# Kernel tuning notes

Measured on AMD Instinct MI355X. Metric: run time of the kernel, lower is better.

The kernel has to match this reference:

```python
import jax, jax.numpy as jnp
import numpy as np

N_NODES = 100000
N_EDGES = 600000
D_FEAT = 128
N_CLASSES = 40
K = 2


def setup_inputs() -> dict:
    key = jax.random.key(0)
    k1, k2, k3, k4, k5 = jax.random.split(key, 5)
    x = jax.random.normal(k1, (N_NODES, D_FEAT), dtype=jnp.float32)
    edge_index = jax.random.randint(k2, (2, N_EDGES), 0, N_NODES, dtype=jnp.int64)
    W = jax.random.normal(k3, (N_CLASSES, D_FEAT), dtype=jnp.float32) / np.sqrt(D_FEAT)
    b = jax.random.normal(k4, (N_CLASSES,), dtype=jnp.float32) * 0.01
    return {"x": x, "edge_index": edge_index, "W": W, "b": b}


def _gcn_norm(edge_index, num_nodes):
    # add self loops (PyG gcn_norm default), edge_weight = 1
    loop = jnp.arange(num_nodes, dtype=edge_index.dtype)
    src = jnp.concatenate([edge_index[0], loop])
    dst = jnp.concatenate([edge_index[1], loop])
    w = jnp.ones(src.shape[0], dtype=jnp.float32)
    deg = jax.ops.segment_sum(w, dst, num_segments=num_nodes)  # [N]
    dinv = jnp.where(deg > 0, 1.0 / jnp.sqrt(deg), 0.0)
    norm = dinv[src] * w * dinv[dst]  # D^-1/2 A_hat D^-1/2 edge weights
    return src, dst, norm


def reference(x, edge_index, W, b):
    # eval mode: dropout is identity
    src, dst, norm = _gcn_norm(edge_index, N_NODES)
    for _ in range(K):
        # message: x_j * norm, aggr='add' at target nodes
        x = jax.ops.segment_sum(x[src] * norm[:, None], dst, num_segments=N_NODES)
    logits = x @ W.T + b  # [N, C]
    return jax.nn.log_softmax(logits, axis=1)
```

## Files before the change

kernel.cpp:

```cpp
#include <hip/hip_runtime.h>

#define N_NODES   100000
#define N_EDGES   600000
#define D_FEAT    128
#define N_CLASSES 40
#define USTRIDE   64

#define NPAD      100352
#define SCAN_NBLK (NPAD / 1024)
#define N_TILES   (N_NODES / 16)
#define G_GEMM    ((N_TILES + 3) / 4)
#define G_FILL    ((N_EDGES + 255) / 256)
#define G_ZERO    (NPAD / 4 / 256 + 1)

typedef __attribute__((ext_vector_type(8))) short bf16x8;
typedef __attribute__((ext_vector_type(4))) float f32x4;

__device__ __forceinline__ float bf2f(unsigned int h) { return __uint_as_float(h << 16); }
__device__ __forceinline__ unsigned int f2bf(float f) {
    unsigned int u = __float_as_uint(f);
    return (u + 0x7FFFu + ((u >> 16) & 1u)) >> 16;
}
__device__ __forceinline__ float4 up4(uint2 v) {
    return make_float4(bf2f(v.x & 0xFFFFu), bf2f(v.x >> 16),
                       bf2f(v.y & 0xFFFFu), bf2f(v.y >> 16));
}
__device__ __forceinline__ uint2 pk4(float4 f) {
    uint2 r;
    r.x = f2bf(f.x) | (f2bf(f.y) << 16);
    r.y = f2bf(f.z) | (f2bf(f.w) << 16);
    return r;
}


__global__ void k_zero_wconv(int4* __restrict__ deg4, const float* __restrict__ W,
                             uint4* __restrict__ wfrag) {
    int t = threadIdx.x;
    if (blockIdx.x < G_ZERO - 1) {
        int i = blockIdx.x * 256 + t;
        if (i < NPAD / 4) deg4[i] = make_int4(0, 0, 0, 0);
        return;
    }
    for (int idx = t; idx < 768; idx += 256) {
        int lane = idx & 63;
        int kc   = (idx >> 6) & 3;
        int ct   = idx >> 8;
        int r16  = lane & 15;
        int g    = lane >> 4;
        int j    = ct * 16 + r16;
        uint4 o = make_uint4(0u, 0u, 0u, 0u);
        if (j < N_CLASSES) {
            const float* wr = W + (size_t)j * D_FEAT + kc * 32 + g * 8;
            float4 w0 = *(const float4*)wr;
            float4 w1 = *(const float4*)(wr + 4);
            o.x = f2bf(w0.x) | (f2bf(w0.y) << 16);
            o.y = f2bf(w0.z) | (f2bf(w0.w) << 16);
            o.z = f2bf(w1.x) | (f2bf(w1.y) << 16);
            o.w = f2bf(w1.z) | (f2bf(w1.w) << 16);
        }
        wfrag[idx] = o;
    }
}

__global__ void k_count(const int* __restrict__ edst, int* __restrict__ deg,
                        int* __restrict__ ord) {
    int e = blockIdx.x * blockDim.x + threadIdx.x;
    if (e < N_EDGES) ord[e] = atomicAdd(&deg[edst[e]], 1);
}

__global__ __launch_bounds__(256) void k_scan1(const int* __restrict__ deg,
                                               int* __restrict__ row_ptr,
                                               int* __restrict__ blksum) {
    __shared__ int wsum[4];
    int t = threadIdx.x;
    int lane = t & 63, w = t >> 6;
    int base = blockIdx.x * 1024 + t * 4;
    int4 v = *(const int4*)(deg + base);
    int s0 = v.x, s1 = s0 + v.y, s2 = s1 + v.z, s3 = s2 + v.w;
    int inc = s3;
#pragma unroll
    for (int d = 1; d < 64; d <<= 1) {
        int y = __shfl_up(inc, d, 64);
        if (lane >= d) inc += y;
    }
    if (lane == 63) wsum[w] = inc;
    __syncthreads();
    int woff = 0;
#pragma unroll
    for (int j = 0; j < 3; ++j) woff += (j < w) ? wsum[j] : 0;
    int texcl = woff + inc - s3;
    int4 o;
    o.x = texcl; o.y = texcl + s0; o.z = texcl + s1; o.w = texcl + s2;
    *(int4*)(row_ptr + base) = o;
    if (t == 255) blksum[blockIdx.x] = woff + inc;
}

__global__ __launch_bounds__(256) void k_scan2(const int* __restrict__ deg,
                                               int* __restrict__ row_ptr,
                                               float* __restrict__ dinv,
                                               const int* __restrict__ blksum) {
    __shared__ int s[SCAN_NBLK];
    int t = threadIdx.x;
    int blk = blockIdx.x;
    if (t < SCAN_NBLK) s[t] = blksum[t];
    __syncthreads();
    int off = 0;
    for (int j = 0; j < blk; ++j) off += s[j];
    int base = blk * 1024 + t * 4;
    int4 v = *(int4*)(row_ptr + base);
    v.x += off; v.y += off; v.z += off; v.w += off;
    *(int4*)(row_ptr + base) = v;
    int4 d = *(const int4*)(deg + base);
    float4 di;
    di.x = rsqrtf((float)(d.x + 1));
    di.y = rsqrtf((float)(d.y + 1));
    di.z = rsqrtf((float)(d.z + 1));
    di.w = rsqrtf((float)(d.w + 1));
    *(float4*)(dinv + base) = di;
}


__global__ __launch_bounds__(256) void k_gemm_fill(const float* __restrict__ x,
                                                   const uint4* __restrict__ wfrag,
                                                   const float* __restrict__ dinv,
                                                   unsigned short* __restrict__ y,
                                                   const int* __restrict__ esrc,
                                                   const int* __restrict__ edst,
                                                   const int* __restrict__ ord,
                                                   const int* __restrict__ row_ptr,
                                                   int* __restrict__ csr_src) {
    if (blockIdx.x >= G_GEMM) {
        int e = (blockIdx.x - G_GEMM) * 256 + threadIdx.x;
        if (e < N_EDGES) {
            csr_src[row_ptr[edst[e]] + ord[e]] = esrc[e];
        }
        return;
    }

    int t = threadIdx.x;
    int wid = t >> 6;
    int lane = t & 63;
    int tile = blockIdx.x * 4 + wid;
    if (tile >= N_TILES) return;

    int r16 = lane & 15;
    int g   = lane >> 4;

    bf16x8 bfrag[3][4];
#pragma unroll
    for (int ct = 0; ct < 3; ++ct) {
#pragma unroll
        for (int kc = 0; kc < 4; ++kc) {
            union { uint4 u4; bf16x8 v; } tmp;
            tmp.u4 = wfrag[(ct * 4 + kc) * 64 + lane];
            bfrag[ct][kc] = tmp.v;
        }
    }

    int node_r = tile * 16 + r16;
    const float4* xp = (const float4*)(x + (size_t)node_r * D_FEAT);

    f32x4 z = {0.f, 0.f, 0.f, 0.f};
    f32x4 acc0 = z, acc1 = z, acc2 = z;

#pragma unroll
    for (int kc = 0; kc < 4; ++kc) {
        float4 x0 = xp[kc * 8 + g * 2];
        float4 x1 = xp[kc * 8 + g * 2 + 1];
        union { bf16x8 v; unsigned int u[4]; } a;
        a.u[0] = f2bf(x0.x) | (f2bf(x0.y) << 16);
        a.u[1] = f2bf(x0.z) | (f2bf(x0.w) << 16);
        a.u[2] = f2bf(x1.x) | (f2bf(x1.y) << 16);
        a.u[3] = f2bf(x1.z) | (f2bf(x1.w) << 16);
        acc0 = __builtin_amdgcn_mfma_f32_16x16x32_bf16(bfrag[0][kc], a.v, acc0, 0, 0, 0);
        acc1 = __builtin_amdgcn_mfma_f32_16x16x32_bf16(bfrag[1][kc], a.v, acc1, 0, 0, 0);
        acc2 = __builtin_amdgcn_mfma_f32_16x16x32_bf16(bfrag[2][kc], a.v, acc2, 0, 0, 0);
    }

    int node = tile * 16 + r16;
    float di = dinv[node];
    unsigned short* orow = y + (size_t)node * USTRIDE;

    uint2 s0, s1;
    s0.x = f2bf(acc0[0] * di) | (f2bf(acc0[1] * di) << 16);
    s0.y = f2bf(acc0[2] * di) | (f2bf(acc0[3] * di) << 16);
    *(uint2*)(orow + g * 4) = s0;
    s1.x = f2bf(acc1[0] * di) | (f2bf(acc1[1] * di) << 16);
    s1.y = f2bf(acc1[2] * di) | (f2bf(acc1[3] * di) << 16);
    *(uint2*)(orow + 16 + g * 4) = s1;
    if (g < 2) {
        uint2 s2;
        s2.x = f2bf(acc2[0] * di) | (f2bf(acc2[1] * di) << 16);
        s2.y = f2bf(acc2[2] * di) | (f2bf(acc2[3] * di) << 16);
        *(uint2*)(orow + 32 + g * 4) = s2;
    }
}


__global__ __launch_bounds__(256) void k_gather(const unsigned short* __restrict__ yin,
                                                unsigned short* __restrict__ yout,
                                                const float* __restrict__ dinv,
                                                const int* __restrict__ row_ptr,
                                                const int* __restrict__ csr_src) {
    int t = blockIdx.x * blockDim.x + threadIdx.x;
    int i = t >> 4;
    if (i >= N_NODES) return;
    int sub = t & 1;
    int par = (t >> 1) & 7;
    const uint2* yb = (const uint2*)yin;

    float4 a[5];
    if (par == 0) {
        const uint2* self = yb + (size_t)i * 16 + sub * 5;
#pragma unroll
        for (int r = 0; r < 5; ++r) a[r] = up4(self[r]);
    } else {
#pragma unroll
        for (int r = 0; r < 5; ++r) a[r] = make_float4(0.f, 0.f, 0.f, 0.f);
    }

    int e = row_ptr[i] + par, end = row_ptr[i + 1];
    for (; e < end; e += 8) {
        int s = csr_src[e];
        const uint2* p = yb + (size_t)s * 16 + sub * 5;
        uint2 w[5];
#pragma unroll
        for (int r = 0; r < 5; ++r) w[r] = p[r];
#pragma unroll
        for (int r = 0; r < 5; ++r) {
            float4 v = up4(w[r]);
            a[r].x += v.x; a[r].y += v.y; a[r].z += v.z; a[r].w += v.w;
        }
    }

#pragma unroll
    for (int d = 2; d <= 8; d <<= 1) {
#pragma unroll
        for (int r = 0; r < 5; ++r) {
            a[r].x += __shfl_xor(a[r].x, d); a[r].y += __shfl_xor(a[r].y, d);
            a[r].z += __shfl_xor(a[r].z, d); a[r].w += __shfl_xor(a[r].w, d);
        }
    }

    if (par == 0) {
        float di = dinv[i];
        float s2 = di * di;
        uint2* o = (uint2*)yout + (size_t)i * 16 + sub * 5;
#pragma unroll
        for (int r = 0; r < 5; ++r) {
            o[r] = pk4(make_float4(a[r].x * s2, a[r].y * s2, a[r].z * s2, a[r].w * s2));
        }
    }
}

__global__ __launch_bounds__(256) void k_gather_out(const unsigned short* __restrict__ yin,
                                                    float* __restrict__ out,
                                                    const float* __restrict__ dinv,
                                                    const int* __restrict__ row_ptr,
                                                    const int* __restrict__ csr_src,
                                                    const float* __restrict__ bias) {
    int t = blockIdx.x * blockDim.x + threadIdx.x;
    int i = t >> 4;
    if (i >= N_NODES) return;
    int sub = t & 1;
    int par = (t >> 1) & 7;
    const uint2* yb = (const uint2*)yin;

    float4 a[5];
    if (par == 0) {
        const uint2* self = yb + (size_t)i * 16 + sub * 5;
#pragma unroll
        for (int r = 0; r < 5; ++r) a[r] = up4(self[r]);
    } else {
#pragma unroll
        for (int r = 0; r < 5; ++r) a[r] = make_float4(0.f, 0.f, 0.f, 0.f);
    }

    int e = row_ptr[i] + par, end = row_ptr[i + 1];
    for (; e < end; e += 8) {
        int s = csr_src[e];
        const uint2* p = yb + (size_t)s * 16 + sub * 5;
        uint2 w[5];
#pragma unroll
        for (int r = 0; r < 5; ++r) w[r] = p[r];
#pragma unroll
        for (int r = 0; r < 5; ++r) {
            float4 v = up4(w[r]);
            a[r].x += v.x; a[r].y += v.y; a[r].z += v.z; a[r].w += v.w;
        }
    }

#pragma unroll
    for (int d = 2; d <= 8; d <<= 1) {
#pragma unroll
        for (int r = 0; r < 5; ++r) {
            a[r].x += __shfl_xor(a[r].x, d); a[r].y += __shfl_xor(a[r].y, d);
            a[r].z += __shfl_xor(a[r].z, d); a[r].w += __shfl_xor(a[r].w, d);
        }
    }

    float di = dinv[i];
    const float4* b4 = (const float4*)bias + sub * 5;
    float4 l[5];
    float m = -INFINITY;
#pragma unroll
    for (int r = 0; r < 5; ++r) {
        float4 b = b4[r];
        l[r].x = a[r].x * di + b.x;
        l[r].y = a[r].y * di + b.y;
        l[r].z = a[r].z * di + b.z;
        l[r].w = a[r].w * di + b.w;
        m = fmaxf(m, fmaxf(fmaxf(l[r].x, l[r].y), fmaxf(l[r].z, l[r].w)));
    }
    m = fmaxf(m, __shfl_xor(m, 1));
    float s = 0.f;
#pragma unroll
    for (int r = 0; r < 5; ++r) {
        s += __expf(l[r].x - m) + __expf(l[r].y - m)
           + __expf(l[r].z - m) + __expf(l[r].w - m);
    }
    s += __shfl_xor(s, 1);
    float lse = __logf(s) + m;

    if (par == 0) {
        float4* o = (float4*)out + (size_t)i * 10 + sub * 5;
#pragma unroll
        for (int r = 0; r < 5; ++r) {
            o[r] = make_float4(l[r].x - lse, l[r].y - lse, l[r].z - lse, l[r].w - lse);
        }
    }
}


extern "C" void kernel_launch(void* const* d_in, const int* in_sizes, int n_in,
                              void* d_out, int out_size, void* d_ws, size_t ws_size,
                              hipStream_t stream) {
    const float* x   = (const float*)d_in[0];
    const int*   ei  = (const int*)d_in[1];
    const float* W   = (const float*)d_in[2];
    const float* b   = (const float*)d_in[3];
    float*       out = (float*)d_out;

    const int* esrc = ei;
    const int* edst = ei + N_EDGES;

    int*   deg     = (int*)d_ws;
    int*   row_ptr = deg + NPAD;
    int*   blksum  = row_ptr + NPAD;
    int*   ord     = blksum + 128;
    int*   csr_src = ord + 600064;
    uint4* wfrag   = (uint4*)(csr_src + 600064);
    float* dinv    = (float*)(csr_src + 600064 + 3072);
    unsigned short* u0 = (unsigned short*)(dinv + NPAD);
    unsigned short* u1 = u0 + (size_t)N_NODES * USTRIDE;

    const int B = 256;
    const int gE = G_FILL;
    const int gG = (16 * N_NODES + B - 1) / B;

    k_zero_wconv<<<G_ZERO, B, 0, stream>>>((int4*)deg, W, wfrag);
    k_count<<<gE, B, 0, stream>>>(edst, deg, ord);
    k_scan1<<<SCAN_NBLK, B, 0, stream>>>(deg, row_ptr, blksum);
    k_scan2<<<SCAN_NBLK, B, 0, stream>>>(deg, row_ptr, dinv, blksum);

    k_gemm_fill<<<G_GEMM + G_FILL, B, 0, stream>>>(x, wfrag, dinv, u0,
                                                   esrc, edst, ord, row_ptr, csr_src);

    k_gather    <<<gG, B, 0, stream>>>(u0, u1, dinv, row_ptr, csr_src);
    k_gather_out<<<gG, B, 0, stream>>>(u1, out, dinv, row_ptr, csr_src, b);
}
```

Baseline: 103.7 us.

## Move GEMM before degree scan, fuse with edge counting, scale in fill pass

The x·W^T projection no longer waits for dinv. It now runs in the same launch as the atomic degree count and writes unscaled bf16 rows to a new buffer. A later pass fuses the CSR fill with scaling those rows by dinv into the gather input. The aim is to overlap the compute-heavy GEMM with the latency-bound atomic counting. The cost is an extra read and write of the projected feature matrix, one more workspace buffer, and a second bf16 rounding.

```diff
diff --git a/kernel.cpp b/kernel.cpp
--- a/kernel.cpp
+++ b/kernel.cpp
@@ -10,7 +10,8 @@
 #define SCAN_NBLK (NPAD / 1024)
 #define N_TILES   (N_NODES / 16)
 #define G_GEMM    ((N_TILES + 3) / 4)
-#define G_FILL    ((N_EDGES + 255) / 256)
+#define G_EDGE    ((N_EDGES + 255) / 256)
+#define G_SCALE   ((N_NODES * 16 + 255) / 256)
 #define G_ZERO    (NPAD / 4 / 256 + 1)
 
 typedef __attribute__((ext_vector_type(8))) short bf16x8;
@@ -62,10 +63,77 @@
     }
 }
 
-__global__ void k_count(const int* __restrict__ edst, int* __restrict__ deg,
-                        int* __restrict__ ord) {
-    int e = blockIdx.x * blockDim.x + threadIdx.x;
-    if (e < N_EDGES) ord[e] = atomicAdd(&deg[edst[e]], 1);
+
+__global__ __launch_bounds__(256) void k_gemm_count(const float* __restrict__ x,
+                                                    const uint4* __restrict__ wfrag,
+                                                    unsigned short* __restrict__ y0,
+                                                    const int* __restrict__ edst,
+                                                    int* __restrict__ deg,
+                                                    int* __restrict__ ord) {
+    if (blockIdx.x >= G_GEMM) {
+        int e = (blockIdx.x - G_GEMM) * 256 + threadIdx.x;
+        if (e < N_EDGES) ord[e] = atomicAdd(&deg[edst[e]], 1);
+        return;
+    }
+
+    int t = threadIdx.x;
+    int wid = t >> 6;
+    int lane = t & 63;
+    int tile = blockIdx.x * 4 + wid;
+    if (tile >= N_TILES) return;
+
+    int r16 = lane & 15;
+    int g   = lane >> 4;
+
+    uint4 wq[12];
+#pragma unroll
+    for (int f = 0; f < 12; ++f) wq[f] = wfrag[f * 64 + lane];
+
+    int node = tile * 16 + r16;
+    const float4* xp = (const float4*)(x + (size_t)node * D_FEAT);
+    float4 xv[8];
+#pragma unroll
+    for (int kc = 0; kc < 4; ++kc) {
+        xv[kc * 2]     = xp[kc * 8 + g * 2];
+        xv[kc * 2 + 1] = xp[kc * 8 + g * 2 + 1];
+    }
+
+    bf16x8 afrag[4];
+#pragma unroll
+    for (int kc = 0; kc < 4; ++kc) {
+        union { bf16x8 v; unsigned int u[4]; } a;
+        a.u[0] = f2bf(xv[kc * 2].x) | (f2bf(xv[kc * 2].y) << 16);
+        a.u[1] = f2bf(xv[kc * 2].z) | (f2bf(xv[kc * 2].w) << 16);
+        a.u[2] = f2bf(xv[kc * 2 + 1].x) | (f2bf(xv[kc * 2 + 1].y) << 16);
+        a.u[3] = f2bf(xv[kc * 2 + 1].z) | (f2bf(xv[kc * 2 + 1].w) << 16);
+        afrag[kc] = a.v;
+    }
+
+    f32x4 z = {0.f, 0.f, 0.f, 0.f};
+    f32x4 acc0 = z, acc1 = z, acc2 = z;
+#pragma unroll
+    for (int kc = 0; kc < 4; ++kc) {
+        union { uint4 u4; bf16x8 v; } b0, b1, b2;
+        b0.u4 = wq[kc];  b1.u4 = wq[4 + kc];  b2.u4 = wq[8 + kc];
+        acc0 = __builtin_amdgcn_mfma_f32_16x16x32_bf16(b0.v, afrag[kc], acc0, 0, 0, 0);
+        acc1 = __builtin_amdgcn_mfma_f32_16x16x32_bf16(b1.v, afrag[kc], acc1, 0, 0, 0);
+        acc2 = __builtin_amdgcn_mfma_f32_16x16x32_bf16(b2.v, afrag[kc], acc2, 0, 0, 0);
+    }
+
+    unsigned short* orow = y0 + (size_t)node * USTRIDE;
+    uint2 s0, s1;
+    s0.x = f2bf(acc0[0]) | (f2bf(acc0[1]) << 16);
+    s0.y = f2bf(acc0[2]) | (f2bf(acc0[3]) << 16);
+    *(uint2*)(orow + g * 4) = s0;
+    s1.x = f2bf(acc1[0]) | (f2bf(acc1[1]) << 16);
+    s1.y = f2bf(acc1[2]) | (f2bf(acc1[3]) << 16);
+    *(uint2*)(orow + 16 + g * 4) = s1;
+    if (g < 2) {
+        uint2 s2;
+        s2.x = f2bf(acc2[0]) | (f2bf(acc2[1]) << 16);
+        s2.y = f2bf(acc2[2]) | (f2bf(acc2[3]) << 16);
+        *(uint2*)(orow + 32 + g * 4) = s2;
+    }
 }
 
 __global__ __launch_bounds__(256) void k_scan1(const int* __restrict__ deg,
@@ -120,80 +188,29 @@
 }
 
 
-__global__ __launch_bounds__(256) void k_gemm_fill(const float* __restrict__ x,
-                                                   const uint4* __restrict__ wfrag,
-                                                   const float* __restrict__ dinv,
-                                                   unsigned short* __restrict__ y,
-                                                   const int* __restrict__ esrc,
-                                                   const int* __restrict__ edst,
-                                                   const int* __restrict__ ord,
-                                                   const int* __restrict__ row_ptr,
-                                                   int* __restrict__ csr_src) {
-    if (blockIdx.x >= G_GEMM) {
-        int e = (blockIdx.x - G_GEMM) * 256 + threadIdx.x;
-        if (e < N_EDGES) {
-            csr_src[row_ptr[edst[e]] + ord[e]] = esrc[e];
-        }
+__global__ __launch_bounds__(256) void k_fill_scale(const int* __restrict__ esrc,
+                                                    const int* __restrict__ edst,
+                                                    const int* __restrict__ ord,
+                                                    const int* __restrict__ row_ptr,
+                                                    int* __restrict__ csr_src,
+                                                    const unsigned short* __restrict__ y0,
+                                                    unsigned short* __restrict__ u0,
+                                                    const float* __restrict__ dinv) {
+    int t = threadIdx.x;
+    if (blockIdx.x < G_EDGE) {
+        int e = blockIdx.x * 256 + t;
+        if (e < N_EDGES) csr_src[row_ptr[edst[e]] + ord[e]] = esrc[e];
         return;
     }
-
-    int t = threadIdx.x;
-    int wid = t >> 6;
-    int lane = t & 63;
-    int tile = blockIdx.x * 4 + wid;
-    if (tile >= N_TILES) return;
-
-    int r16 = lane & 15;
-    int g   = lane >> 4;
-
-    bf16x8 bfrag[3][4];
-#pragma unroll
-    for (int ct = 0; ct < 3; ++ct) {
-#pragma unroll
-        for (int kc = 0; kc < 4; ++kc) {
-            union { uint4 u4; bf16x8 v; } tmp;
-            tmp.u4 = wfrag[(ct * 4 + kc) * 64 + lane];
-            bfrag[ct][kc] = tmp.v;
-        }
-    }
-
-    int node_r = tile * 16 + r16;
-    const float4* xp = (const float4*)(x + (size_t)node_r * D_FEAT);
-
-    f32x4 z = {0.f, 0.f, 0.f, 0.f};
-    f32x4 acc0 = z, acc1 = z, acc2 = z;
-
-#pragma unroll
-    for (int kc = 0; kc < 4; ++kc) {
-        float4 x0 = xp[kc * 8 + g * 2];
-        float4 x1 = xp[kc * 8 + g * 2 + 1];
-        union { bf16x8 v; unsigned int u[4]; } a;
-        a.u[0] = f2bf(x0.x) | (f2bf(x0.y) << 16);
-        a.u[1] = f2bf(x0.z) | (f2bf(x0.w) << 16);
-        a.u[2] = f2bf(x1.x) | (f2bf(x1.y) << 16);
-        a.u[3] = f2bf(x1.z) | (f2bf(x1.w) << 16);
-        acc0 = __builtin_amdgcn_mfma_f32_16x16x32_bf16(bfrag[0][kc], a.v, acc0, 0, 0, 0);
-        acc1 = __builtin_amdgcn_mfma_f32_16x16x32_bf16(bfrag[1][kc], a.v, acc1, 0, 0, 0);
-        acc2 = __builtin_amdgcn_mfma_f32_16x16x32_bf16(bfrag[2][kc], a.v, acc2, 0, 0, 0);
-    }
-
-    int node = tile * 16 + r16;
+    int idx = (blockIdx.x - G_EDGE) * 256 + t;
+    if (idx >= N_NODES * 16) return;
+    int node = idx >> 4;
+    int slot = idx & 15;
+    if (slot >= 10) return;
     float di = dinv[node];
-    unsigned short* orow = y + (size_t)node * USTRIDE;
-
-    uint2 s0, s1;
-    s0.x = f2bf(acc0[0] * di) | (f2bf(acc0[1] * di) << 16);
-    s0.y = f2bf(acc0[2] * di) | (f2bf(acc0[3] * di) << 16);
-    *(uint2*)(orow + g * 4) = s0;
-    s1.x = f2bf(acc1[0] * di) | (f2bf(acc1[1] * di) << 16);
-    s1.y = f2bf(acc1[2] * di) | (f2bf(acc1[3] * di) << 16);
-    *(uint2*)(orow + 16 + g * 4) = s1;
-    if (g < 2) {
-        uint2 s2;
-        s2.x = f2bf(acc2[0] * di) | (f2bf(acc2[1] * di) << 16);
-        s2.y = f2bf(acc2[2] * di) | (f2bf(acc2[3] * di) << 16);
-        *(uint2*)(orow + 32 + g * 4) = s2;
-    }
+    uint2 v = ((const uint2*)y0)[idx];
+    float4 f = up4(v);
+    ((uint2*)u0)[idx] = pk4(make_float4(f.x * di, f.y * di, f.z * di, f.w * di));
 }
 
 
@@ -351,21 +368,19 @@
     int*   csr_src = ord + 600064;
     uint4* wfrag   = (uint4*)(csr_src + 600064);
     float* dinv    = (float*)(csr_src + 600064 + 3072);
-    unsigned short* u0 = (unsigned short*)(dinv + NPAD);
+    unsigned short* y0 = (unsigned short*)(dinv + NPAD);
+    unsigned short* u0 = y0 + (size_t)N_NODES * USTRIDE;
     unsigned short* u1 = u0 + (size_t)N_NODES * USTRIDE;
 
     const int B = 256;
-    const int gE = G_FILL;
     const int gG = (16 * N_NODES + B - 1) / B;
 
     k_zero_wconv<<<G_ZERO, B, 0, stream>>>((int4*)deg, W, wfrag);
-    k_count<<<gE, B, 0, stream>>>(edst, deg, ord);
+    k_gemm_count<<<G_GEMM + G_EDGE, B, 0, stream>>>(x, wfrag, y0, edst, deg, ord);
     k_scan1<<<SCAN_NBLK, B, 0, stream>>>(deg, row_ptr, blksum);
     k_scan2<<<SCAN_NBLK, B, 0, stream>>>(deg, row_ptr, dinv, blksum);
-
-    k_gemm_fill<<<G_GEMM + G_FILL, B, 0, stream>>>(x, wfrag, dinv, u0,
-                                                   esrc, edst, ord, row_ptr, csr_src);
-
+    k_fill_scale<<<G_EDGE + G_SCALE, B, 0, stream>>>(esrc, edst, ord, row_ptr,
+                                                     csr_src, y0, u0, dinv);
     k_gather    <<<gG, B, 0, stream>>>(u0, u1, dinv, row_ptr, csr_src);
     k_gather_out<<<gG, B, 0, stream>>>(u1, out, dinv, row_ptr, csr_src, b);
 }
```

Result: slower. 106.8 us (+3.0%).
